# Performance work log

Hardware: AMD Instinct MI355X
Metric: run time of the kernel (lower is better)

The kernel has to match this reference:

```python
import jax, jax.numpy as jnp
import numpy as np

N = 100000
E = 1600000
F_IN = 128
F_HID = 64


def setup_inputs() -> dict:
    key = jax.random.key(0)
    ks = jax.random.split(key, 8)
    x = jax.random.normal(ks[0], (N, F_IN), dtype=jnp.float32)
    edge_index = jax.random.randint(ks[1], (2, E), 0, N, dtype=jnp.int64)
    # GCNConv params (PyG default: weight, then bias added after aggregation)
    s1 = 1.0 / np.sqrt(F_IN)
    s2 = 1.0 / np.sqrt(F_HID)
    W1 = jax.random.uniform(ks[2], (F_IN, F_HID), jnp.float32, -s1, s1)
    b1 = jnp.zeros((F_HID,), jnp.float32)
    W2 = jax.random.uniform(ks[3], (F_HID, F_HID), jnp.float32, -s2, s2)
    b2 = jnp.zeros((F_HID,), jnp.float32)
    # Linear(hidden, 1) for predict_link
    Wout = jax.random.uniform(ks[4], (F_HID, 1), jnp.float32, -s2, s2)
    bout = jax.random.uniform(ks[5], (1,), jnp.float32, -s2, s2)
    return {"x": x, "edge_index": edge_index, "W1": W1, "b1": b1,
            "W2": W2, "b2": b2, "Wout": Wout, "bout": bout}


def _gcn_conv(x, row, col, W, b):
    # x: [N, Fin]; row/col: [E'] (self-loops already appended)
    h = x @ W                                              # [N, Fout]
    deg = jax.ops.segment_sum(jnp.ones_like(col, dtype=h.dtype), col,
                              num_segments=N)              # [N]
    dinv = jnp.where(deg > 0, jax.lax.rsqrt(jnp.maximum(deg, 1e-12)), 0.0)
    norm = dinv[row] * dinv[col]                           # [E']
    msg = h[row] * norm[:, None]                           # [E', Fout]
    out = jax.ops.segment_sum(msg, col, num_segments=N)    # [N, Fout]
    return out + b


def reference(x, edge_index, W1, b1, W2, b2, Wout, bout):
    row0, col0 = edge_index[0], edge_index[1]
    # add self-loops (GCNConv default)
    loop = jnp.arange(N, dtype=edge_index.dtype)
    row = jnp.concatenate([row0, loop])
    col = jnp.concatenate([col0, loop])

    h = jax.nn.relu(_gcn_conv(x, row, col, W1, b1))   # dropout p=0.0 (eval)
    h = jax.nn.relu(_gcn_conv(h, row, col, W2, b2))

    # predict_link on the original (no-self-loop) edges
    edge_features = h[row0] * h[col0]                 # [E, F_HID]
    return edge_features @ Wout + bout                # [E, 1]
```

## Files before the change

kernel.cpp:

```cpp
#include <hip/hip_runtime.h>

#define NN 100000
#define EE 1600000
#define FIN 128
#define FHID 64

#define BSH 7
#define NB  ((NN + 127) / 128)
#define CAP 3072
#define BIN_BLOCKS 256
#define BIN_EPT 8
#define BIN_EPB (1024 * BIN_EPT)

typedef union { _Float16 h[4]; uint2 u; } H4;
typedef union { _Float16 h[8]; uint4 u; } H8;
typedef union { _Float16 h[16]; uint4 u[2]; } H16;

__global__ void k_zero_int(int* __restrict__ p, int n) {
    int i = blockIdx.x * blockDim.x + threadIdx.x;
    if (i < n) p[i] = 0;
}

__global__ __launch_bounds__(1024) void k_bin(const int* __restrict__ row,
                                              const int* __restrict__ col,
                                              int* __restrict__ bcnt,
                                              unsigned long long* __restrict__ rec) {
    __shared__ int hist[NB];
    __shared__ int base[NB];
    int tid = threadIdx.x;
    for (int i = tid; i < NB; i += 1024) hist[i] = 0;
    __syncthreads();
    int e0 = blockIdx.x * BIN_EPB;
    int b[BIN_EPT];
    int rnk[BIN_EPT];
    unsigned long long pk[BIN_EPT];
#pragma unroll
    for (int j = 0; j < BIN_EPT; ++j) {
        int e = e0 + j * 1024 + tid;
        b[j] = -1;
        if (e < EE) {
            int c = col[e];
            int r = row[e];
            b[j] = c >> BSH;
            pk[j] = ((unsigned long long)(unsigned)c << 32) | (unsigned)r;
            rnk[j] = atomicAdd(&hist[b[j]], 1);
        }
    }
    __syncthreads();
    for (int i = tid; i < NB; i += 1024) {
        int h = hist[i];
        base[i] = h ? atomicAdd(&bcnt[i], h) : 0;
    }
    __syncthreads();
#pragma unroll
    for (int j = 0; j < BIN_EPT; ++j) {
        if (b[j] >= 0) {
            int p = base[b[j]] + rnk[j];
            if (p < CAP) rec[(size_t)b[j] * CAP + p] = pk[j];
        }
    }
}

__global__ __launch_bounds__(1024) void k_scanb(const int* __restrict__ bcnt,
                                                int* __restrict__ bbase) {
    __shared__ int s[1024];
    int t = threadIdx.x;
    int v = (t < NB) ? bcnt[t] : 0;
    s[t] = v;
    __syncthreads();
    for (int off = 1; off < 1024; off <<= 1) {
        int x = (t >= off) ? s[t - off] : 0;
        __syncthreads();
        s[t] += x;
        __syncthreads();
    }
    if (t < NB) bbase[t] = s[t] - v;
}

__global__ __launch_bounds__(256) void k_csr(const int* __restrict__ bcnt,
                                             const int* __restrict__ bbase,
                                             const unsigned long long* __restrict__ rec,
                                             int* __restrict__ csr_src,
                                             int* __restrict__ starts,
                                             int* __restrict__ degi,
                                             float* __restrict__ dinv) {
    __shared__ unsigned short rank[CAP];
    __shared__ int nh[128];
    __shared__ int ns[128];
    __shared__ int nsx[128];
    int b = blockIdx.x;
    int tid = threadIdx.x;
    int cnt = bcnt[b];
    if (cnt > CAP) cnt = CAP;
    int gb = bbase[b];
    const unsigned long long* r = rec + (size_t)b * CAP;
    if (tid < 128) nh[tid] = 0;
    __syncthreads();
    for (int i = tid; i < cnt; i += 256) {
        int c = (int)(r[i] >> 32);
        int cl = c - (b << BSH);
        rank[i] = (unsigned short)atomicAdd(&nh[cl], 1);
    }
    __syncthreads();
    if (tid < 128) ns[tid] = nh[tid];
    __syncthreads();
    for (int off = 1; off < 128; off <<= 1) {
        int x = 0;
        if (tid < 128 && tid >= off) x = ns[tid - off];
        __syncthreads();
        if (tid < 128) ns[tid] += x;
        __syncthreads();
    }
    if (tid < 128) {
        int excl = ns[tid] - nh[tid];
        nsx[tid] = excl;
        int n = (b << BSH) + tid;
        if (n < NN) {
            starts[n] = gb + excl;
            degi[n] = nh[tid];
            dinv[n] = rsqrtf((float)(nh[tid] + 1));
        }
    }
    __syncthreads();
    for (int i = tid; i < cnt; i += 256) {
        unsigned long long rv = r[i];
        int c = (int)(rv >> 32);
        int cl = c - (b << BSH);
        csr_src[gb + nsx[cl] + (int)rank[i]] = (int)(rv & 0xffffffffu);
    }
}

#define XPAD 129
__global__ __launch_bounds__(256) void k_gemm1(const float* __restrict__ x,
                                               const float* __restrict__ W1,
                                               const float* __restrict__ dinv,
                                               uint4* __restrict__ hs16) {
    __shared__ float xl[64 * XPAD];
    int tid = threadIdx.x;
    int n0 = blockIdx.x * 64;
    const float4* x4 = reinterpret_cast<const float4*>(x);
#pragma unroll
    for (int i = 0; i < 8; ++i) {
        int idx = i * 256 + tid;
        int row = idx >> 5;
        int k4 = idx & 31;
        float4 v = {0.f, 0.f, 0.f, 0.f};
        if (n0 + row < NN) v = x4[(size_t)(n0 + row) * 32 + k4];
        float* p = &xl[row * XPAD + k4];
        p[0] = v.x; p[32] = v.y; p[64] = v.z; p[96] = v.w;
    }
    __syncthreads();

    int wv = __builtin_amdgcn_readfirstlane(tid >> 6);
    int lane = tid & 63;
    float acc[16];
#pragma unroll
    for (int c = 0; c < 16; ++c) acc[c] = 0.f;
    const float* Wb = W1 + wv * 16;
    const float* xrow = &xl[lane * XPAD];
#pragma unroll 8
    for (int k = 0; k < FIN; ++k) {
        float xk = xrow[((k & 3) << 5) | (k >> 2)];
        const float* wr = Wb + k * FHID;
#pragma unroll
        for (int c = 0; c < 16; ++c) acc[c] = fmaf(xk, wr[c], acc[c]);
    }

    int node = n0 + lane;
    if (node < NN) {
        float dn = dinv[node];
        H16 pk;
#pragma unroll
        for (int c = 0; c < 16; ++c) pk.h[c] = (_Float16)(acc[c] * dn);
        hs16[(size_t)node * 8 + wv * 2] = pk.u[0];
        hs16[(size_t)node * 8 + wv * 2 + 1] = pk.u[1];
    }
}

#define X2PAD 65
__global__ __launch_bounds__(256) void k_gemm2(const uint2* __restrict__ y1,
                                               const float* __restrict__ W2,
                                               const float* __restrict__ dinv,
                                               uint4* __restrict__ hs16) {
    __shared__ float al[64 * X2PAD];
    int tid = threadIdx.x;
    int n0 = blockIdx.x * 64;
#pragma unroll
    for (int i = 0; i < 4; ++i) {
        int idx = i * 256 + tid;
        int row = idx >> 4;
        int k4 = idx & 15;
        float4 v = {0.f, 0.f, 0.f, 0.f};
        if (n0 + row < NN) {
            H4 t;
            t.u = y1[(size_t)(n0 + row) * 16 + k4];
            v.x = (float)t.h[0]; v.y = (float)t.h[1];
            v.z = (float)t.h[2]; v.w = (float)t.h[3];
        }
        float* p = &al[row * X2PAD + k4];
        p[0] = v.x; p[16] = v.y; p[32] = v.z; p[48] = v.w;
    }
    __syncthreads();

    int wv = __builtin_amdgcn_readfirstlane(tid >> 6);
    int lane = tid & 63;
    float acc[16];
#pragma unroll
    for (int c = 0; c < 16; ++c) acc[c] = 0.f;
    const float* Wb = W2 + wv * 16;
    const float* arow = &al[lane * X2PAD];
#pragma unroll 8
    for (int k = 0; k < FHID; ++k) {
        float xk = arow[((k & 3) << 4) | (k >> 2)];
        const float* wr = Wb + k * FHID;
#pragma unroll
        for (int c = 0; c < 16; ++c) acc[c] = fmaf(xk, wr[c], acc[c]);
    }

    int node = n0 + lane;
    if (node < NN) {
        float dn = dinv[node];
        H16 pk;
#pragma unroll
        for (int c = 0; c < 16; ++c) pk.h[c] = (_Float16)(acc[c] * dn);
        hs16[(size_t)node * 8 + wv * 2] = pk.u[0];
        hs16[(size_t)node * 8 + wv * 2 + 1] = pk.u[1];
    }
}

__global__ __launch_bounds__(256) void k_gath(const int* __restrict__ starts,
                                              const int* __restrict__ degi,
                                              const int* __restrict__ csr_src,
                                              const float* __restrict__ dinv,
                                              const uint4* __restrict__ hIn,
                                              const float* __restrict__ bias,
                                              uint4* __restrict__ yOut) {
    int wave = threadIdx.x >> 6;
    int lane = threadIdx.x & 63;
    int g = lane >> 3;
    int fl = lane & 7;
    int n = blockIdx.x * 4 + wave;
    if (n >= NN) return;
    int s = starts[n];
    int d = degi[n];
    float a[8];
    H8 pk;
    if (g == 0) {
        pk.u = hIn[(size_t)n * 8 + fl];
#pragma unroll
        for (int j = 0; j < 8; ++j) a[j] = (float)pk.h[j];
    } else {
#pragma unroll
        for (int j = 0; j < 8; ++j) a[j] = 0.f;
    }
    int k = g;
    for (; k + 8 < d; k += 16) {
        int r0 = csr_src[s + k];
        int r1 = csr_src[s + k + 8];
        H8 v0, v1;
        v0.u = hIn[(size_t)r0 * 8 + fl];
        v1.u = hIn[(size_t)r1 * 8 + fl];
#pragma unroll
        for (int j = 0; j < 8; ++j) a[j] += (float)v0.h[j] + (float)v1.h[j];
    }
    if (k < d) {
        int r = csr_src[s + k];
        pk.u = hIn[(size_t)r * 8 + fl];
#pragma unroll
        for (int j = 0; j < 8; ++j) a[j] += (float)pk.h[j];
    }
#pragma unroll
    for (int j = 0; j < 8; ++j) {
        a[j] += __shfl_xor(a[j], 8);
        a[j] += __shfl_xor(a[j], 16);
        a[j] += __shfl_xor(a[j], 32);
    }
    if (g == 0) {
        float dn = dinv[n];
        float4 b0 = reinterpret_cast<const float4*>(bias)[fl * 2];
        float4 b1 = reinterpret_cast<const float4*>(bias)[fl * 2 + 1];
        H8 o;
        o.h[0] = (_Float16)fmaxf(fmaf(a[0], dn, b0.x), 0.f);
        o.h[1] = (_Float16)fmaxf(fmaf(a[1], dn, b0.y), 0.f);
        o.h[2] = (_Float16)fmaxf(fmaf(a[2], dn, b0.z), 0.f);
        o.h[3] = (_Float16)fmaxf(fmaf(a[3], dn, b0.w), 0.f);
        o.h[4] = (_Float16)fmaxf(fmaf(a[4], dn, b1.x), 0.f);
        o.h[5] = (_Float16)fmaxf(fmaf(a[5], dn, b1.y), 0.f);
        o.h[6] = (_Float16)fmaxf(fmaf(a[6], dn, b1.z), 0.f);
        o.h[7] = (_Float16)fmaxf(fmaf(a[7], dn, b1.w), 0.f);
        yOut[(size_t)n * 8 + fl] = o.u;
    }
}

__global__ __launch_bounds__(256) void k_link(const int* __restrict__ row0,
                                              const int* __restrict__ col0,
                                              const uint4* __restrict__ y16,
                                              const float* __restrict__ Wout,
                                              const float* __restrict__ bout,
                                              float* __restrict__ out) {
    int wid = blockIdx.x * 4 + (threadIdx.x >> 6);
    int lane = threadIdx.x & 63;
    int sub = lane >> 3;
    int fl = lane & 7;
    float4 w0 = reinterpret_cast<const float4*>(Wout)[fl * 2];
    float4 w1 = reinterpret_cast<const float4*>(Wout)[fl * 2 + 1];
    float wv[8] = {w0.x, w0.y, w0.z, w0.w, w1.x, w1.y, w1.z, w1.w};
    float bout0 = bout[0];
    const int NO = EE / 8;
    int stride = gridDim.x * 4;
    for (int q = wid; q < NO; q += stride) {
        int e = q * 8 + sub;
        int r = row0[e];
        int c = col0[e];
        H8 hr, hc;
        hr.u = y16[(size_t)r * 8 + fl];
        hc.u = y16[(size_t)c * 8 + fl];
        float p = 0.f;
#pragma unroll
        for (int j = 0; j < 8; ++j)
            p = fmaf((float)hr.h[j], (float)hc.h[j] * wv[j], p);
        p += __shfl_xor(p, 1);
        p += __shfl_xor(p, 2);
        p += __shfl_xor(p, 4);
        if (fl == 0) out[e] = p + bout0;
    }
}

extern "C" void kernel_launch(void* const* d_in, const int* in_sizes, int n_in,
                              void* d_out, int out_size, void* d_ws, size_t ws_size,
                              hipStream_t stream) {
    const float* x    = (const float*)d_in[0];
    const int*   ei   = (const int*)d_in[1];
    const float* W1   = (const float*)d_in[2];
    const float* b1   = (const float*)d_in[3];
    const float* W2   = (const float*)d_in[4];
    const float* b2   = (const float*)d_in[5];
    const float* Wout = (const float*)d_in[6];
    const float* bout = (const float*)d_in[7];
    const int*   row0 = ei;
    const int*   col0 = ei + EE;

    char* ws = (char*)d_ws;
    auto align = [](size_t v) { return (v + 255) / 256 * 256; };
    const size_t nInt = align((size_t)NN * 4);
    float* dinv    = (float*)ws;                 ws += nInt;
    int*   degi    = (int*)ws;                   ws += nInt;
    int*   starts  = (int*)ws;                   ws += nInt;
    int*   bcnt    = (int*)ws;                   ws += align((size_t)NB * 4);
    int*   bbase   = (int*)ws;                   ws += align((size_t)NB * 4);
    int*   csr_src = (int*)ws;                   ws += align((size_t)EE * 4);
    uint4* bufH    = (uint4*)ws;                 ws += align((size_t)NN * FHID * 2);
    uint4* bufY    = (uint4*)ws;                 ws += align((size_t)NN * FHID * 2);
    unsigned long long* rec = (unsigned long long*)bufH;
    float* out = (float*)d_out;

    const int nTiles = (NN + 63) / 64;

    k_zero_int<<<(NB + 255) / 256, 256, 0, stream>>>(bcnt, NB);
    k_bin<<<BIN_BLOCKS, 1024, 0, stream>>>(row0, col0, bcnt, rec);
    k_scanb<<<1, 1024, 0, stream>>>(bcnt, bbase);
    k_csr<<<NB, 256, 0, stream>>>(bcnt, bbase, rec, csr_src, starts, degi, dinv);

    k_gemm1<<<nTiles, 256, 0, stream>>>(x, W1, dinv, bufH);
    k_gath<<<(NN + 3) / 4, 256, 0, stream>>>(starts, degi, csr_src, dinv, bufH, b1, bufY);

    k_gemm2<<<nTiles, 256, 0, stream>>>((const uint2*)bufY, W2, dinv, bufH);
    k_gath<<<(NN + 3) / 4, 256, 0, stream>>>(starts, degi, csr_src, dinv, bufH, b2, bufY);

    k_link<<<2048, 256, 0, stream>>>(row0, col0, bufY, Wout, bout, out);
}
```

Baseline: 216.2 us.

## Fuse edge binning with first GEMM, drop scan, and compute link scores per destination

Binning and the first feature GEMM now run as one launch: some blocks bin edges into fixed-capacity per-bucket slots while the other blocks compute x@W1. Because the GEMM no longer waits for degrees, the dinv scaling of the source side moves into the first gather. The global scan kernel is removed by giving each bucket a fixed CAP-sized region of the CSR arrays. The CSR also records the original edge id, so the link prediction runs per destination node. It loads that node's hidden row once and reuses it across all its incoming edges, writing scores scattered by edge id. The packed record uses 17/21-bit fields, which only holds for these N and E values. Output writes become scattered.

After: 246.3 us. 13.9% more time.

```diff
diff --git a/kernel.cpp b/kernel.cpp
--- a/kernel.cpp
+++ b/kernel.cpp
@@ -8,9 +8,8 @@
 #define BSH 7
 #define NB  ((NN + 127) / 128)
 #define CAP 3072
-#define BIN_BLOCKS 256
+#define BINB NB
 #define BIN_EPT 8
-#define BIN_EPB (1024 * BIN_EPT)
 
 typedef union { _Float16 h[4]; uint2 u; } H4;
 typedef union { _Float16 h[8]; uint4 u; } H8;
@@ -21,66 +20,96 @@
     if (i < n) p[i] = 0;
 }
 
-__global__ __launch_bounds__(1024) void k_bin(const int* __restrict__ row,
-                                              const int* __restrict__ col,
-                                              int* __restrict__ bcnt,
-                                              unsigned long long* __restrict__ rec) {
-    __shared__ int hist[NB];
-    __shared__ int base[NB];
+#define XPAD 129
+
+__global__ __launch_bounds__(256) void k_fused(const int* __restrict__ row,
+                                               const int* __restrict__ col,
+                                               int* __restrict__ bcnt,
+                                               unsigned long long* __restrict__ rec,
+                                               const float* __restrict__ x,
+                                               const float* __restrict__ W1,
+                                               uint4* __restrict__ hs16) {
+    __shared__ float smem[64 * XPAD];
     int tid = threadIdx.x;
-    for (int i = tid; i < NB; i += 1024) hist[i] = 0;
-    __syncthreads();
-    int e0 = blockIdx.x * BIN_EPB;
-    int b[BIN_EPT];
-    int rnk[BIN_EPT];
-    unsigned long long pk[BIN_EPT];
-#pragma unroll
-    for (int j = 0; j < BIN_EPT; ++j) {
-        int e = e0 + j * 1024 + tid;
-        b[j] = -1;
-        if (e < EE) {
-            int c = col[e];
-            int r = row[e];
-            b[j] = c >> BSH;
-            pk[j] = ((unsigned long long)(unsigned)c << 32) | (unsigned)r;
-            rnk[j] = atomicAdd(&hist[b[j]], 1);
-        }
-    }
-    __syncthreads();
-    for (int i = tid; i < NB; i += 1024) {
-        int h = hist[i];
-        base[i] = h ? atomicAdd(&bcnt[i], h) : 0;
-    }
-    __syncthreads();
-#pragma unroll
-    for (int j = 0; j < BIN_EPT; ++j) {
-        if (b[j] >= 0) {
-            int p = base[b[j]] + rnk[j];
-            if (p < CAP) rec[(size_t)b[j] * CAP + p] = pk[j];
-        }
-    }
-}
-
-__global__ __launch_bounds__(1024) void k_scanb(const int* __restrict__ bcnt,
-                                                int* __restrict__ bbase) {
-    __shared__ int s[1024];
-    int t = threadIdx.x;
-    int v = (t < NB) ? bcnt[t] : 0;
-    s[t] = v;
-    __syncthreads();
-    for (int off = 1; off < 1024; off <<= 1) {
-        int x = (t >= off) ? s[t - off] : 0;
-        __syncthreads();
-        s[t] += x;
-        __syncthreads();
-    }
-    if (t < NB) bbase[t] = s[t] - v;
+    if (blockIdx.x < BINB) {
+        int* hist = (int*)smem;
+        int* base = hist + NB;
+        for (int i = tid; i < NB; i += 256) hist[i] = 0;
+        __syncthreads();
+        int e0 = blockIdx.x * (256 * BIN_EPT);
+        int b[BIN_EPT];
+        int rnk[BIN_EPT];
+        unsigned long long pk[BIN_EPT];
+#pragma unroll
+        for (int j = 0; j < BIN_EPT; ++j) {
+            int e = e0 + j * 256 + tid;
+            b[j] = -1;
+            if (e < EE) {
+                int c = col[e];
+                int r = row[e];
+                b[j] = c >> BSH;
+                pk[j] = ((unsigned long long)(unsigned)c << 38) |
+                        ((unsigned long long)(unsigned)r << 21) |
+                        (unsigned long long)(unsigned)e;
+                rnk[j] = atomicAdd(&hist[b[j]], 1);
+            }
+        }
+        __syncthreads();
+        for (int i = tid; i < NB; i += 256) {
+            int h = hist[i];
+            base[i] = h ? atomicAdd(&bcnt[i], h) : 0;
+        }
+        __syncthreads();
+#pragma unroll
+        for (int j = 0; j < BIN_EPT; ++j) {
+            if (b[j] >= 0) {
+                int p = base[b[j]] + rnk[j];
+                if (p < CAP) rec[(size_t)b[j] * CAP + p] = pk[j];
+            }
+        }
+    } else {
+        int n0 = (blockIdx.x - BINB) * 64;
+        const float4* x4 = reinterpret_cast<const float4*>(x);
+#pragma unroll
+        for (int i = 0; i < 8; ++i) {
+            int idx = i * 256 + tid;
+            int rw = idx >> 5;
+            int k4 = idx & 31;
+            float4 v = {0.f, 0.f, 0.f, 0.f};
+            if (n0 + rw < NN) v = x4[(size_t)(n0 + rw) * 32 + k4];
+            float* p = &smem[rw * XPAD + k4];
+            p[0] = v.x; p[32] = v.y; p[64] = v.z; p[96] = v.w;
+        }
+        __syncthreads();
+        int wv = __builtin_amdgcn_readfirstlane(tid >> 6);
+        int lane = tid & 63;
+        float acc[16];
+#pragma unroll
+        for (int c = 0; c < 16; ++c) acc[c] = 0.f;
+        const float* Wb = W1 + wv * 16;
+        const float* xrow = &smem[lane * XPAD];
+#pragma unroll 8
+        for (int k = 0; k < FIN; ++k) {
+            float xk = xrow[((k & 3) << 5) | (k >> 2)];
+            const float* wr = Wb + k * FHID;
+#pragma unroll
+            for (int c = 0; c < 16; ++c) acc[c] = fmaf(xk, wr[c], acc[c]);
+        }
+        int node = n0 + lane;
+        if (node < NN) {
+            H16 pk2;
+#pragma unroll
+            for (int c = 0; c < 16; ++c) pk2.h[c] = (_Float16)acc[c];
+            hs16[(size_t)node * 8 + wv * 2] = pk2.u[0];
+            hs16[(size_t)node * 8 + wv * 2 + 1] = pk2.u[1];
+        }
+    }
 }
 
 __global__ __launch_bounds__(256) void k_csr(const int* __restrict__ bcnt,
-                                             const int* __restrict__ bbase,
                                              const unsigned long long* __restrict__ rec,
                                              int* __restrict__ csr_src,
+                                             int* __restrict__ csr_eid,
                                              int* __restrict__ starts,
                                              int* __restrict__ degi,
                                              float* __restrict__ dinv) {
@@ -92,12 +121,12 @@
     int tid = threadIdx.x;
     int cnt = bcnt[b];
     if (cnt > CAP) cnt = CAP;
-    int gb = bbase[b];
+    int gb = b * CAP;
     const unsigned long long* r = rec + (size_t)b * CAP;
     if (tid < 128) nh[tid] = 0;
     __syncthreads();
     for (int i = tid; i < cnt; i += 256) {
-        int c = (int)(r[i] >> 32);
+        int c = (int)(r[i] >> 38);
         int cl = c - (b << BSH);
         rank[i] = (unsigned short)atomicAdd(&nh[cl], 1);
     }
@@ -124,56 +153,11 @@
     __syncthreads();
     for (int i = tid; i < cnt; i += 256) {
         unsigned long long rv = r[i];
-        int c = (int)(rv >> 32);
+        int c = (int)(rv >> 38);
         int cl = c - (b << BSH);
-        csr_src[gb + nsx[cl] + (int)rank[i]] = (int)(rv & 0xffffffffu);
-    }
-}
-
-#define XPAD 129
-__global__ __launch_bounds__(256) void k_gemm1(const float* __restrict__ x,
-                                               const float* __restrict__ W1,
-                                               const float* __restrict__ dinv,
-                                               uint4* __restrict__ hs16) {
-    __shared__ float xl[64 * XPAD];
-    int tid = threadIdx.x;
-    int n0 = blockIdx.x * 64;
-    const float4* x4 = reinterpret_cast<const float4*>(x);
-#pragma unroll
-    for (int i = 0; i < 8; ++i) {
-        int idx = i * 256 + tid;
-        int row = idx >> 5;
-        int k4 = idx & 31;
-        float4 v = {0.f, 0.f, 0.f, 0.f};
-        if (n0 + row < NN) v = x4[(size_t)(n0 + row) * 32 + k4];
-        float* p = &xl[row * XPAD + k4];
-        p[0] = v.x; p[32] = v.y; p[64] = v.z; p[96] = v.w;
-    }
-    __syncthreads();
-
-    int wv = __builtin_amdgcn_readfirstlane(tid >> 6);
-    int lane = tid & 63;
-    float acc[16];
-#pragma unroll
-    for (int c = 0; c < 16; ++c) acc[c] = 0.f;
-    const float* Wb = W1 + wv * 16;
-    const float* xrow = &xl[lane * XPAD];
-#pragma unroll 8
-    for (int k = 0; k < FIN; ++k) {
-        float xk = xrow[((k & 3) << 5) | (k >> 2)];
-        const float* wr = Wb + k * FHID;
-#pragma unroll
-        for (int c = 0; c < 16; ++c) acc[c] = fmaf(xk, wr[c], acc[c]);
-    }
-
-    int node = n0 + lane;
-    if (node < NN) {
-        float dn = dinv[node];
-        H16 pk;
-#pragma unroll
-        for (int c = 0; c < 16; ++c) pk.h[c] = (_Float16)(acc[c] * dn);
-        hs16[(size_t)node * 8 + wv * 2] = pk.u[0];
-        hs16[(size_t)node * 8 + wv * 2 + 1] = pk.u[1];
+        int pos = gb + nsx[cl] + (int)rank[i];
+        csr_src[pos] = (int)((rv >> 21) & 0x1FFFF);
+        csr_eid[pos] = (int)(rv & 0x1FFFFF);
     }
 }
 
@@ -188,16 +172,16 @@
 #pragma unroll
     for (int i = 0; i < 4; ++i) {
         int idx = i * 256 + tid;
-        int row = idx >> 4;
+        int rw = idx >> 4;
         int k4 = idx & 15;
         float4 v = {0.f, 0.f, 0.f, 0.f};
-        if (n0 + row < NN) {
+        if (n0 + rw < NN) {
             H4 t;
-            t.u = y1[(size_t)(n0 + row) * 16 + k4];
+            t.u = y1[(size_t)(n0 + rw) * 16 + k4];
             v.x = (float)t.h[0]; v.y = (float)t.h[1];
             v.z = (float)t.h[2]; v.w = (float)t.h[3];
         }
-        float* p = &al[row * X2PAD + k4];
+        float* p = &al[rw * X2PAD + k4];
         p[0] = v.x; p[16] = v.y; p[32] = v.z; p[48] = v.w;
     }
     __syncthreads();
@@ -228,6 +212,7 @@
     }
 }
 
+template <int SCALED>
 __global__ __launch_bounds__(256) void k_gath(const int* __restrict__ starts,
                                               const int* __restrict__ degi,
                                               const int* __restrict__ csr_src,
@@ -247,8 +232,9 @@
     H8 pk;
     if (g == 0) {
         pk.u = hIn[(size_t)n * 8 + fl];
-#pragma unroll
-        for (int j = 0; j < 8; ++j) a[j] = (float)pk.h[j];
+        float dm = SCALED ? 1.f : dinv[n];
+#pragma unroll
+        for (int j = 0; j < 8; ++j) a[j] = (float)pk.h[j] * dm;
     } else {
 #pragma unroll
         for (int j = 0; j < 8; ++j) a[j] = 0.f;
@@ -260,14 +246,24 @@
         H8 v0, v1;
         v0.u = hIn[(size_t)r0 * 8 + fl];
         v1.u = hIn[(size_t)r1 * 8 + fl];
-#pragma unroll
-        for (int j = 0; j < 8; ++j) a[j] += (float)v0.h[j] + (float)v1.h[j];
+        if (SCALED) {
+#pragma unroll
+            for (int j = 0; j < 8; ++j) a[j] += (float)v0.h[j] + (float)v1.h[j];
+        } else {
+            float d0 = dinv[r0], d1 = dinv[r1];
+#pragma unroll
+            for (int j = 0; j < 8; ++j) {
+                a[j] = fmaf((float)v0.h[j], d0, a[j]);
+                a[j] = fmaf((float)v1.h[j], d1, a[j]);
+            }
+        }
     }
     if (k < d) {
         int r = csr_src[s + k];
         pk.u = hIn[(size_t)r * 8 + fl];
-#pragma unroll
-        for (int j = 0; j < 8; ++j) a[j] += (float)pk.h[j];
+        float dm = SCALED ? 1.f : dinv[r];
+#pragma unroll
+        for (int j = 0; j < 8; ++j) a[j] = fmaf((float)pk.h[j], dm, a[j]);
     }
 #pragma unroll
     for (int j = 0; j < 8; ++j) {
@@ -292,33 +288,63 @@
     }
 }
 
-__global__ __launch_bounds__(256) void k_link(const int* __restrict__ row0,
-                                              const int* __restrict__ col0,
-                                              const uint4* __restrict__ y16,
-                                              const float* __restrict__ Wout,
-                                              const float* __restrict__ bout,
-                                              float* __restrict__ out) {
-    int wid = blockIdx.x * 4 + (threadIdx.x >> 6);
+__global__ __launch_bounds__(256) void k_linkc(const int* __restrict__ starts,
+                                               const int* __restrict__ degi,
+                                               const int* __restrict__ csr_src,
+                                               const int* __restrict__ csr_eid,
+                                               const uint4* __restrict__ y16,
+                                               const float* __restrict__ Wout,
+                                               const float* __restrict__ bout,
+                                               float* __restrict__ out) {
+    int wave = threadIdx.x >> 6;
     int lane = threadIdx.x & 63;
-    int sub = lane >> 3;
+    int g = lane >> 3;
     int fl = lane & 7;
+    int n = blockIdx.x * 4 + wave;
+    if (n >= NN) return;
+    int d = degi[n];
+    if (d == 0) return;
+    int s = starts[n];
+    H8 yc;
+    yc.u = y16[(size_t)n * 8 + fl];
     float4 w0 = reinterpret_cast<const float4*>(Wout)[fl * 2];
     float4 w1 = reinterpret_cast<const float4*>(Wout)[fl * 2 + 1];
-    float wv[8] = {w0.x, w0.y, w0.z, w0.w, w1.x, w1.y, w1.z, w1.w};
+    float cw[8] = {(float)yc.h[0] * w0.x, (float)yc.h[1] * w0.y,
+                   (float)yc.h[2] * w0.z, (float)yc.h[3] * w0.w,
+                   (float)yc.h[4] * w1.x, (float)yc.h[5] * w1.y,
+                   (float)yc.h[6] * w1.z, (float)yc.h[7] * w1.w};
     float bout0 = bout[0];
-    const int NO = EE / 8;
-    int stride = gridDim.x * 4;
-    for (int q = wid; q < NO; q += stride) {
-        int e = q * 8 + sub;
-        int r = row0[e];
-        int c = col0[e];
-        H8 hr, hc;
-        hr.u = y16[(size_t)r * 8 + fl];
-        hc.u = y16[(size_t)c * 8 + fl];
+    int k = g;
+    for (; k + 8 < d; k += 16) {
+        int r0 = csr_src[s + k];
+        int r1 = csr_src[s + k + 8];
+        int e0 = csr_eid[s + k];
+        int e1 = csr_eid[s + k + 8];
+        H8 v0, v1;
+        v0.u = y16[(size_t)r0 * 8 + fl];
+        v1.u = y16[(size_t)r1 * 8 + fl];
+        float p0 = 0.f, p1 = 0.f;
+#pragma unroll
+        for (int j = 0; j < 8; ++j) {
+            p0 = fmaf((float)v0.h[j], cw[j], p0);
+            p1 = fmaf((float)v1.h[j], cw[j], p1);
+        }
+        p0 += __shfl_xor(p0, 1); p1 += __shfl_xor(p1, 1);
+        p0 += __shfl_xor(p0, 2); p1 += __shfl_xor(p1, 2);
+        p0 += __shfl_xor(p0, 4); p1 += __shfl_xor(p1, 4);
+        if (fl == 0) {
+            out[e0] = p0 + bout0;
+            out[e1] = p1 + bout0;
+        }
+    }
+    if (k < d) {
+        int r = csr_src[s + k];
+        int e = csr_eid[s + k];
+        H8 v;
+        v.u = y16[(size_t)r * 8 + fl];
         float p = 0.f;
 #pragma unroll
-        for (int j = 0; j < 8; ++j)
-            p = fmaf((float)hr.h[j], (float)hc.h[j] * wv[j], p);
+        for (int j = 0; j < 8; ++j) p = fmaf((float)v.h[j], cw[j], p);
         p += __shfl_xor(p, 1);
         p += __shfl_xor(p, 2);
         p += __shfl_xor(p, 4);
@@ -347,25 +373,25 @@
     int*   degi    = (int*)ws;                   ws += nInt;
     int*   starts  = (int*)ws;                   ws += nInt;
     int*   bcnt    = (int*)ws;                   ws += align((size_t)NB * 4);
-    int*   bbase   = (int*)ws;                   ws += align((size_t)NB * 4);
-    int*   csr_src = (int*)ws;                   ws += align((size_t)EE * 4);
+    int*   csr_src = (int*)ws;                   ws += align((size_t)NB * CAP * 4);
+    int*   csr_eid = (int*)ws;                   ws += align((size_t)NB * CAP * 4);
+    unsigned long long* rec = (unsigned long long*)ws;
+    ws += align((size_t)NB * CAP * 8);
     uint4* bufH    = (uint4*)ws;                 ws += align((size_t)NN * FHID * 2);
     uint4* bufY    = (uint4*)ws;                 ws += align((size_t)NN * FHID * 2);
-    unsigned long long* rec = (unsigned long long*)bufH;
     float* out = (float*)d_out;
 
     const int nTiles = (NN + 63) / 64;
 
     k_zero_int<<<(NB + 255) / 256, 256, 0, stream>>>(bcnt, NB);
-    k_bin<<<BIN_BLOCKS, 1024, 0, stream>>>(row0, col0, bcnt, rec);
-    k_scanb<<<1, 1024, 0, stream>>>(bcnt, bbase);
-    k_csr<<<NB, 256, 0, stream>>>(bcnt, bbase, rec, csr_src, starts, degi, dinv);
-
-    k_gemm1<<<nTiles, 256, 0, stream>>>(x, W1, dinv, bufH);
-    k_gath<<<(NN + 3) / 4, 256, 0, stream>>>(starts, degi, csr_src, dinv, bufH, b1, bufY);
+    k_fused<<<BINB + nTiles, 256, 0, stream>>>(row0, col0, bcnt, rec, x, W1, bufH);
+    k_csr<<<NB, 256, 0, stream>>>(bcnt, rec, csr_src, csr_eid, starts, degi, dinv);
+
+    k_gath<0><<<(NN + 3) / 4, 256, 0, stream>>>(starts, degi, csr_src, dinv, bufH, b1, bufY);
 
     k_gemm2<<<nTiles, 256, 0, stream>>>((const uint2*)bufY, W2, dinv, bufH);
-    k_gath<<<(NN + 3) / 4, 256, 0, stream>>>(starts, degi, csr_src, dinv, bufH, b2, bufY);
-
-    k_link<<<2048, 256, 0, stream>>>(row0, col0, bufY, Wout, bout, out);
-}
+    k_gath<1><<<(NN + 3) / 4, 256, 0, stream>>>(starts, degi, csr_src, dinv, bufH, b2, bufY);
+
+    k_linkc<<<(NN + 3) / 4, 256, 0, stream>>>(starts, degi, csr_src, csr_eid,
+                                              bufY, Wout, bout, out);
+}
```

## Drop bucket scan with padded CSR and preload neighbor indices via shuffles

Applied to the files above, without the earlier changes.

Removes the single-block prefix-scan kernel by giving each bucket a fixed CAP-sized slot in the CSR array, which leaves gaps but saves one launch. The gather kernel now loads up to 64 neighbor indices in one coalesced read per wave and broadcasts them with shuffles instead of issuing per-group index loads. It also packs edge records with a 17-bit shift. This changes the gather loop from a two-way unrolled form to one load per iteration, which may reduce memory-level parallelism.

Result: no change. 215.1 us (-0.5%).

```diff
diff --git a/kernel.cpp b/kernel.cpp
--- a/kernel.cpp
+++ b/kernel.cpp
@@ -42,7 +42,7 @@
             int c = col[e];
             int r = row[e];
             b[j] = c >> BSH;
-            pk[j] = ((unsigned long long)(unsigned)c << 32) | (unsigned)r;
+            pk[j] = ((unsigned long long)(unsigned)c << 17) | (unsigned)r;
             rnk[j] = atomicAdd(&hist[b[j]], 1);
         }
     }
@@ -61,24 +61,7 @@
     }
 }
 
-__global__ __launch_bounds__(1024) void k_scanb(const int* __restrict__ bcnt,
-                                                int* __restrict__ bbase) {
-    __shared__ int s[1024];
-    int t = threadIdx.x;
-    int v = (t < NB) ? bcnt[t] : 0;
-    s[t] = v;
-    __syncthreads();
-    for (int off = 1; off < 1024; off <<= 1) {
-        int x = (t >= off) ? s[t - off] : 0;
-        __syncthreads();
-        s[t] += x;
-        __syncthreads();
-    }
-    if (t < NB) bbase[t] = s[t] - v;
-}
-
 __global__ __launch_bounds__(256) void k_csr(const int* __restrict__ bcnt,
-                                             const int* __restrict__ bbase,
                                              const unsigned long long* __restrict__ rec,
                                              int* __restrict__ csr_src,
                                              int* __restrict__ starts,
@@ -92,12 +75,12 @@
     int tid = threadIdx.x;
     int cnt = bcnt[b];
     if (cnt > CAP) cnt = CAP;
-    int gb = bbase[b];
+    int gb = b * CAP;
     const unsigned long long* r = rec + (size_t)b * CAP;
     if (tid < 128) nh[tid] = 0;
     __syncthreads();
     for (int i = tid; i < cnt; i += 256) {
-        int c = (int)(r[i] >> 32);
+        int c = (int)(r[i] >> 17);
         int cl = c - (b << BSH);
         rank[i] = (unsigned short)atomicAdd(&nh[cl], 1);
     }
@@ -124,9 +107,9 @@
     __syncthreads();
     for (int i = tid; i < cnt; i += 256) {
         unsigned long long rv = r[i];
-        int c = (int)(rv >> 32);
+        int c = (int)(rv >> 17);
         int cl = c - (b << BSH);
-        csr_src[gb + nsx[cl] + (int)rank[i]] = (int)(rv & 0xffffffffu);
+        csr_src[gb + nsx[cl] + (int)rank[i]] = (int)(rv & 0x1FFFF);
     }
 }
 
@@ -188,16 +171,16 @@
 #pragma unroll
     for (int i = 0; i < 4; ++i) {
         int idx = i * 256 + tid;
-        int row = idx >> 4;
+        int rw = idx >> 4;
         int k4 = idx & 15;
         float4 v = {0.f, 0.f, 0.f, 0.f};
-        if (n0 + row < NN) {
+        if (n0 + rw < NN) {
             H4 t;
-            t.u = y1[(size_t)(n0 + row) * 16 + k4];
+            t.u = y1[(size_t)(n0 + rw) * 16 + k4];
             v.x = (float)t.h[0]; v.y = (float)t.h[1];
             v.z = (float)t.h[2]; v.w = (float)t.h[3];
         }
-        float* p = &al[row * X2PAD + k4];
+        float* p = &al[rw * X2PAD + k4];
         p[0] = v.x; p[16] = v.y; p[32] = v.z; p[48] = v.w;
     }
     __syncthreads();
@@ -243,6 +226,7 @@
     if (n >= NN) return;
     int s = starts[n];
     int d = degi[n];
+    int idx = (lane < d) ? csr_src[s + lane] : 0;
     float a[8];
     H8 pk;
     if (g == 0) {
@@ -253,21 +237,20 @@
 #pragma unroll
         for (int j = 0; j < 8; ++j) a[j] = 0.f;
     }
-    int k = g;
-    for (; k + 8 < d; k += 16) {
-        int r0 = csr_src[s + k];
-        int r1 = csr_src[s + k + 8];
-        H8 v0, v1;
-        v0.u = hIn[(size_t)r0 * 8 + fl];
-        v1.u = hIn[(size_t)r1 * 8 + fl];
-#pragma unroll
-        for (int j = 0; j < 8; ++j) a[j] += (float)v0.h[j] + (float)v1.h[j];
-    }
-    if (k < d) {
+    int dc = d < 64 ? d : 64;
+    for (int k = g; k < dc; k += 8) {
+        int r = __shfl(idx, k);
+        H8 v;
+        v.u = hIn[(size_t)r * 8 + fl];
+#pragma unroll
+        for (int j = 0; j < 8; ++j) a[j] += (float)v.h[j];
+    }
+    for (int k = 64 + g; k < d; k += 8) {
         int r = csr_src[s + k];
-        pk.u = hIn[(size_t)r * 8 + fl];
-#pragma unroll
-        for (int j = 0; j < 8; ++j) a[j] += (float)pk.h[j];
+        H8 v;
+        v.u = hIn[(size_t)r * 8 + fl];
+#pragma unroll
+        for (int j = 0; j < 8; ++j) a[j] += (float)v.h[j];
     }
 #pragma unroll
     for (int j = 0; j < 8; ++j) {
@@ -347,8 +330,7 @@
     int*   degi    = (int*)ws;                   ws += nInt;
     int*   starts  = (int*)ws;                   ws += nInt;
     int*   bcnt    = (int*)ws;                   ws += align((size_t)NB * 4);
-    int*   bbase   = (int*)ws;                   ws += align((size_t)NB * 4);
-    int*   csr_src = (int*)ws;                   ws += align((size_t)EE * 4);
+    int*   csr_src = (int*)ws;                   ws += align((size_t)NB * CAP * 4);
     uint4* bufH    = (uint4*)ws;                 ws += align((size_t)NN * FHID * 2);
     uint4* bufY    = (uint4*)ws;                 ws += align((size_t)NN * FHID * 2);
     unsigned long long* rec = (unsigned long long*)bufH;
@@ -358,8 +340,7 @@
 
     k_zero_int<<<(NB + 255) / 256, 256, 0, stream>>>(bcnt, NB);
     k_bin<<<BIN_BLOCKS, 1024, 0, stream>>>(row0, col0, bcnt, rec);
-    k_scanb<<<1, 1024, 0, stream>>>(bcnt, bbase);
-    k_csr<<<NB, 256, 0, stream>>>(bcnt, bbase, rec, csr_src, starts, degi, dinv);
+    k_csr<<<NB, 256, 0, stream>>>(bcnt, rec, csr_src, starts, degi, dinv);
 
     k_gemm1<<<nTiles, 256, 0, stream>>>(x, W1, dinv, bufH);
     k_gath<<<(NN + 3) / 4, 256, 0, stream>>>(starts, degi, csr_src, dinv, bufH, b1, bufY);
```
